# Kernel optimization log

Measured on AMD Instinct MI355X. Metric: run time of the kernel, lower is better.

The kernel has to match this reference:

```python
import math
import jax, jax.numpy as jnp
import numpy as np

NUM_ANGLE = 8
NUM_RADIAL = 3
RADIAL_MIN = 0.08
RADIAL_MAX = 0.9
EPS = 1e-6


def _hann(n):
    # torch.hann_window(n, periodic=False)
    return 0.5 * (1.0 - jnp.cos(2.0 * jnp.pi * jnp.arange(n, dtype=jnp.float32) / (n - 1)))


def _to_luma(img):
    # img: [B, 3, H, W] -> [B, H, W]
    return 0.2989 * img[:, 0] + 0.587 * img[:, 1] + 0.114 * img[:, 2]


def _log_magnitude(img):
    x = _to_luma(img).astype(jnp.float32)  # [B, H, W]
    H, W = x.shape[-2], x.shape[-1]
    win = _hann(H)[:, None] * _hann(W)[None, :]  # [H, W]
    x = x * win
    spec = jnp.fft.fftshift(jnp.fft.fft2(x, axes=(-2, -1)), axes=(-2, -1))
    return jnp.log1p(jnp.abs(spec))  # [B, H, W]


def _polar_masks(H, W):
    y = jnp.linspace(-1.0, 1.0, H, dtype=jnp.float32)
    x = jnp.linspace(-1.0, 1.0, W, dtype=jnp.float32)
    yy, xx = jnp.meshgrid(y, x, indexing='ij')
    radius = jnp.sqrt(xx * xx + yy * yy)
    radius = radius / jnp.maximum(radius.max(), EPS)
    angle = jnp.remainder(jnp.arctan2(yy, xx), math.pi)

    r_edges = jnp.linspace(RADIAL_MIN, RADIAL_MAX, NUM_RADIAL + 1, dtype=jnp.float32)
    a_edges = jnp.linspace(0.0, math.pi, NUM_ANGLE + 1, dtype=jnp.float32)

    r0 = r_edges[:-1][:, None, None]
    r1 = r_edges[1:][:, None, None]
    rmask = (radius[None] >= r0) & (radius[None] < r1)           # [R, H, W]
    rmask = rmask.at[-1].set((radius >= r_edges[-2]) & (radius <= r_edges[-1]))

    t0 = a_edges[:-1][:, None, None]
    t1 = a_edges[1:][:, None, None]
    amask = (angle[None] >= t0) & (angle[None] < t1)             # [A, H, W]
    amask = amask.at[-1].set((angle >= a_edges[-2]) & (angle <= a_edges[-1]))

    return (rmask[:, None] & amask[None, :]).astype(jnp.float32)  # [R, A, H, W]


def _sector_energies(img):
    mag = _log_magnitude(img)                          # [B, H, W]
    masks = _polar_masks(mag.shape[-2], mag.shape[-1])  # [R, A, H, W]
    mask_sum = jnp.maximum(masks.sum(axis=(-2, -1)), EPS)        # [R, A]
    masked_sum = jnp.einsum('bhw,rahw->bra', mag, masks)         # [B, R, A]
    energies = masked_sum / mask_sum[None]
    energies = energies / jnp.maximum(energies.sum(axis=-1, keepdims=True), EPS)
    return energies


def setup_inputs() -> dict:
    key = jax.random.key(0)
    k1, k2 = jax.random.split(key)
    B, C, H, W = 16, 3, 512, 512
    prediction = jax.random.uniform(k1, (B, C, H, W), dtype=jnp.float32)
    target = jax.random.uniform(k2, (B, C, H, W), dtype=jnp.float32)
    radial_weights = jnp.array([0.5, 1.0, 1.2], dtype=jnp.float32).reshape(1, NUM_RADIAL, 1)
    return {"prediction": prediction, "target": target, "radial_weights": radial_weights}


def reference(prediction, target, radial_weights):
    pred_e = _sector_energies(prediction)   # [B, R, A]
    tgt_e = _sector_energies(target)
    diff = pred_e - tgt_e
    dist = jnp.sqrt(diff * diff + EPS)      # charbonnier
    return (dist * radial_weights).mean()
```

## Files before the change

kernel.cpp:

```cpp
#include <hip/hip_runtime.h>
#include <math.h>

#define PI_F 3.14159265358979323846f
#define TWO_PI_F 6.28318530717958647692f
#define RSQ2 0.70710678118654752440f

#define LGKM(n) __asm__ volatile("s_waitcnt lgkmcnt(" #n ")" ::: "memory")
#define LADDR(a) ((a) + ((a) >> 3))

__device__ __forceinline__ float2 cadd(float2 a, float2 b){ return make_float2(a.x+b.x, a.y+b.y); }
__device__ __forceinline__ float2 csub(float2 a, float2 b){ return make_float2(a.x-b.x, a.y-b.y); }
__device__ __forceinline__ float2 cmul(float2 a, float2 b){ return make_float2(a.x*b.x - a.y*b.y, a.x*b.y + a.y*b.x); }
__device__ __forceinline__ float2 cw1(float2 a){ return make_float2(RSQ2*(a.x+a.y), RSQ2*(a.y-a.x)); }
__device__ __forceinline__ float2 cw2(float2 a){ return make_float2(a.y, -a.x); }
__device__ __forceinline__ float2 cw3(float2 a){ return make_float2(RSQ2*(a.y-a.x), -RSQ2*(a.x+a.y)); }

__device__ __forceinline__ void dft8(float2* v){
    float2 a0=cadd(v[0],v[4]), a1=cadd(v[1],v[5]), a2=cadd(v[2],v[6]), a3=cadd(v[3],v[7]);
    float2 b0=csub(v[0],v[4]);
    float2 b1=cw1(csub(v[1],v[5]));
    float2 b2=cw2(csub(v[2],v[6]));
    float2 b3=cw3(csub(v[3],v[7]));
    float2 c0=cadd(a0,a2), c2=csub(a0,a2), c1=cadd(a1,a3), c3=cw2(csub(a1,a3));
    float2 d0=cadd(b0,b2), d2=csub(b0,b2), d1=cadd(b1,b3), d3=cw2(csub(b1,b3));
    v[0]=cadd(c0,c1); v[1]=csub(c0,c1);
    v[2]=cadd(c2,c3); v[3]=csub(c2,c3);
    v[4]=cadd(d0,d1); v[5]=csub(d0,d1);
    v[6]=cadd(d2,d3); v[7]=csub(d2,d3);
}

__device__ __forceinline__ void calc_pows(float2 w, float2* p){
    p[0] = w;
    p[1] = cmul(w, w);
    p[2] = cmul(p[1], w);
    p[3] = cmul(p[1], p[1]);
    p[4] = cmul(p[2], p[1]);
    p[5] = cmul(p[2], p[2]);
    p[6] = cmul(p[3], p[2]);
}

__device__ __forceinline__ void stage_store(float2* wl, const float2* v, const float2* p,
                                            int base, int step){
    constexpr int br[8] = {0,4,2,6,1,5,3,7};
    wl[LADDR(base)] = v[0];
    #pragma unroll
    for (int c = 1; c < 8; ++c) wl[LADDR(base + step*c)] = cmul(v[br[c]], p[c-1]);
}

__device__ __forceinline__ void stage_load(const float2* wl, float2* v, int j){
    #pragma unroll
    for (int i = 0; i < 8; ++i) v[i] = wl[LADDR(j + 64*i)];
}

__device__ __forceinline__ int sector_id(int hm, int wm) {
    const float step = 2.0f / 511.0f;
    float y = -1.0f + step * (float)hm;
    float x = -1.0f + step * (float)wm;
    float radius = sqrtf(x * x + y * y);
    float r = radius / sqrtf(2.0f);
    float a = atan2f(y, x);
    a = fmodf(a, PI_F);
    if (a < 0.0f) a += PI_F;

    const float rstep = (0.9f - 0.08f) / 3.0f;
    const float re0 = 0.08f;
    const float re1 = 0.08f + rstep;
    const float re2 = 0.08f + 2.0f * rstep;
    const float re3 = 0.9f;
    int rb;
    if      (r >= re0 && r < re1)  rb = 0;
    else if (r >= re1 && r < re2)  rb = 1;
    else if (r >= re2 && r <= re3) rb = 2;
    else return -1;

    const float astep = PI_F / 8.0f;
    int ab = 7;
    #pragma unroll
    for (int i = 0; i < 7; ++i) {
        float t0 = astep * (float)i;
        float t1 = astep * (float)(i + 1);
        if (a >= t0 && a < t1) { ab = i; break; }
    }
    return rb * 8 + ab;
}

__device__ __forceinline__ float hannf(int i) {
    return 0.5f * (1.0f - __cosf(TWO_PI_F * (float)i / 511.0f));
}

__device__ __forceinline__ float lumaf(const float* b, size_t off){
    return 0.2989f*b[off] + 0.587f*b[off+262144] + 0.114f*b[off+524288];
}

__global__ __launch_bounds__(256, 4) void rowfft_kernel(const float* __restrict__ pred,
                                                        const float* __restrict__ tgt,
                                                        float4* __restrict__ out4,
                                                        unsigned char* __restrict__ mapT,
                                                        unsigned short* __restrict__ cnt_u16,
                                                        float* __restrict__ acc_rep) {
    __shared__ float2 lds[4 * 1152];
    __shared__ float cbins[24];
    int blk = blockIdx.x;
    int img = blk >> 5;
    int pb  = blk & 31;
    int t = threadIdx.x;
    int wv = t >> 6, j = t & 63;
    int hpA = pb * 8 + wv * 2;
    int hpB = hpA + 1;
    int h0 = 2 * hpA;
    float2* wlA = lds + wv * 1152;
    float2* wlB = wlA + 576;

    if (blk < 48) acc_rep[blk * 256 + t] = 0.0f;
    if (t < 24) cbins[t] = 0.0f;
    __syncthreads();
    {
        int idx = blk * 256 + t;
        int wm = idx >> 9, hm = idx & 511;
        int s = sector_id(hm, wm);
        mapT[idx] = (unsigned char)(s < 0 ? 255 : s);
        if (s >= 0) atomicAdd(&cbins[s], 1.0f);
    }

    const float* base = (img < 16) ? (pred + (size_t)img * 786432)
                                   : (tgt  + (size_t)(img - 16) * 786432);
    float whA0 = hannf(h0), whA1 = hannf(h0 + 1);
    float whB0 = hannf(h0 + 2), whB1 = hannf(h0 + 3);
    float2 va[8], vb[8];
    #pragma unroll
    for (int i = 0; i < 8; ++i) {
        int w = j + 64 * i;
        float ww = hannf(w);
        size_t off0 = (size_t)h0 * 512 + w;
        float l0 = lumaf(base, off0);
        float l1 = lumaf(base, off0 + 512);
        float l2 = lumaf(base, off0 + 1024);
        float l3 = lumaf(base, off0 + 1536);
        va[i] = make_float2(l0 * (whA0 * ww), l1 * (whA1 * ww));
        vb[i] = make_float2(l2 * (whB0 * ww), l3 * (whB1 * ww));
    }

    float sn, cs;
    __sincosf(-TWO_PI_F * (float)j / 512.0f, &sn, &cs);
    float2 tw0 = make_float2(cs, sn);
    __sincosf(-TWO_PI_F * (float)((j >> 3) << 3) / 512.0f, &sn, &cs);
    float2 tw1 = make_float2(cs, sn);
    float2 pw[7];

    calc_pows(tw0, pw);
    dft8(va);
    dft8(vb);
    stage_store(wlA, va, pw, 8 * j, 1);
    stage_store(wlB, vb, pw, 8 * j, 1);
    LGKM(8);
    stage_load(wlA, va, j);
    LGKM(8);
    stage_load(wlB, vb, j);
    LGKM(8);
    calc_pows(tw1, pw);
    dft8(va);
    stage_store(wlA, va, pw, (j & 7) + 64 * (j >> 3), 8);
    LGKM(8);
    dft8(vb);
    stage_store(wlB, vb, pw, (j & 7) + 64 * (j >> 3), 8);
    LGKM(8);
    stage_load(wlA, va, j);
    LGKM(8);
    stage_load(wlB, vb, j);
    LGKM(8);
    dft8(va);
    LGKM(0);
    dft8(vb);

    constexpr int br[8] = {0,4,2,6,1,5,3,7};
    size_t kbase = (size_t)img * 256;
    int partner = (64 - j) & 63;
    #pragma unroll
    for (int c = 0; c < 4; ++c) {
        int k = j + 64 * c;
        float2 zk = va[br[c]];
        float mx = __shfl(va[br[7 - c]].x, partner, 64);
        float my = __shfl(va[br[7 - c]].y, partner, 64);
        float2 zs = va[br[(8 - c) & 7]];
        float2 zm = make_float2(j == 0 ? zs.x : mx, j == 0 ? zs.y : my);
        float4 o = make_float4(0.5f*(zk.x+zm.x), 0.5f*(zk.y-zm.y),
                               0.5f*(zk.y+zm.y), 0.5f*(zm.x-zk.x));
        if (k != 0) out4[(kbase + (size_t)k) * 256 + hpA] = o;
        zk = vb[br[c]];
        mx = __shfl(vb[br[7 - c]].x, partner, 64);
        my = __shfl(vb[br[7 - c]].y, partner, 64);
        zs = vb[br[(8 - c) & 7]];
        zm = make_float2(j == 0 ? zs.x : mx, j == 0 ? zs.y : my);
        o = make_float4(0.5f*(zk.x+zm.x), 0.5f*(zk.y-zm.y),
                        0.5f*(zk.y+zm.y), 0.5f*(zm.x-zk.x));
        if (k != 0) out4[(kbase + (size_t)k) * 256 + hpB] = o;
    }
    if (j == 0) {
        float2 z0 = va[br[0]], z4 = va[br[4]];
        out4[kbase * 256 + hpA] = make_float4(z0.x, z4.x, z0.y, z4.y);
        z0 = vb[br[0]]; z4 = vb[br[4]];
        out4[kbase * 256 + hpB] = make_float4(z0.x, z4.x, z0.y, z4.y);
    }
    __syncthreads();
    if (t < 24) cnt_u16[t * 1024 + blk] = (unsigned short)(int)cbins[t];
}

__global__ __launch_bounds__(256, 4) void colfft_kernel(const float2* __restrict__ buf,
                                                        const unsigned char* __restrict__ mapT,
                                                        float* __restrict__ acc_rep) {
    __shared__ float2 lds[4 * 1152];
    int t = threadIdx.x;
    int wv = t >> 6, j = t & 63;
    int pg = blockIdx.x * 4 + wv;
    int gidA = pg * 2;
    int img = pg >> 7;
    int wA = gidA & 255, wB = wA + 1;
    float2* wlA = lds + wv * 1152;
    float2* wlB = wlA + 576;

    const float2* colA = buf + (size_t)gidA * 512;
    float2 va[8], vb[8];
    #pragma unroll
    for (int i = 0; i < 8; ++i) va[i] = colA[j + 64 * i];
    #pragma unroll
    for (int i = 0; i < 8; ++i) vb[i] = colA[512 + j + 64 * i];

    bool pairw = (wA == 0);
    const unsigned char* mwA1 = mapT + (size_t)(pairw ? 256 : ((wA + 256) & 511)) * 512;
    const unsigned char* mwA2 = mapT + (size_t)(pairw ? 0   : ((256 - wA) & 511)) * 512;
    const unsigned char* mwB1 = mapT + (size_t)((wB + 256) & 511) * 512;
    const unsigned char* mwB2 = mapT + (size_t)((256 - wB) & 511) * 512;
    unsigned char sA1[8], sA2[8], sB1[8], sB2[8];
    #pragma unroll
    for (int c = 0; c < 8; ++c) {
        int hm = j + 64 * ((c + 4) & 7);
        int hm2 = (256 - (j + 64 * c)) & 511;
        sA1[c] = mwA1[hm];
        sA2[c] = pairw ? mwA2[hm] : mwA2[hm2];
        sB1[c] = mwB1[hm];
        sB2[c] = mwB2[hm2];
    }

    float sn, cs;
    __sincosf(-TWO_PI_F * (float)j / 512.0f, &sn, &cs);
    float2 tw0 = make_float2(cs, sn);
    __sincosf(-TWO_PI_F * (float)((j >> 3) << 3) / 512.0f, &sn, &cs);
    float2 tw1 = make_float2(cs, sn);
    float2 pw[7];

    calc_pows(tw0, pw);
    dft8(va);
    dft8(vb);
    stage_store(wlA, va, pw, 8 * j, 1);
    stage_store(wlB, vb, pw, 8 * j, 1);
    LGKM(8);
    stage_load(wlA, va, j);
    LGKM(8);
    stage_load(wlB, vb, j);
    LGKM(8);
    calc_pows(tw1, pw);
    dft8(va);
    stage_store(wlA, va, pw, (j & 7) + 64 * (j >> 3), 8);
    LGKM(8);
    dft8(vb);
    stage_store(wlB, vb, pw, (j & 7) + 64 * (j >> 3), 8);
    LGKM(8);
    stage_load(wlA, va, j);
    LGKM(8);
    stage_load(wlB, vb, j);
    LGKM(8);
    dft8(va);
    LGKM(0);
    dft8(vb);

    float* wb = (float*)wlA;
    #pragma unroll
    for (int i = 0; i < 4; ++i) { int ii = j + 64 * i; if (ii < 200) wb[ii] = 0.0f; }
    LGKM(0);

    constexpr int br[8] = {0,4,2,6,1,5,3,7};
    int rep = (j & 7) * 25;
    if (pairw) {
        int partner = (64 - j) & 63;
        #pragma unroll
        for (int c = 0; c < 8; ++c) {
            float2 zk = va[br[c]];
            float mx = __shfl(va[br[7 - c]].x, partner, 64);
            float my = __shfl(va[br[7 - c]].y, partner, 64);
            float2 zs = va[br[(8 - c) & 7]];
            float2 zm = make_float2(j == 0 ? zs.x : mx, j == 0 ? zs.y : my);
            float f0x = 0.5f*(zk.x+zm.x), f0y = 0.5f*(zk.y-zm.y);
            float f1x = 0.5f*(zk.y+zm.y), f1y = 0.5f*(zm.x-zk.x);
            float mag0 = __logf(1.0f + sqrtf(f0x*f0x + f0y*f0y));
            float mag1 = __logf(1.0f + sqrtf(f1x*f1x + f1y*f1y));
            int s1 = sA1[c]; if (s1 < 24) atomicAdd(&wb[rep + s1], mag0);
            int s2 = sA2[c]; if (s2 < 24) atomicAdd(&wb[rep + s2], mag1);
        }
    } else {
        #pragma unroll
        for (int c = 0; c < 8; ++c) {
            float2 z = va[br[c]];
            float mag = __logf(1.0f + sqrtf(z.x * z.x + z.y * z.y));
            int s1 = sA1[c]; if (s1 < 24) atomicAdd(&wb[rep + s1], mag);
            int s2 = sA2[c]; if (s2 < 24) atomicAdd(&wb[rep + s2], mag);
        }
    }
    #pragma unroll
    for (int c = 0; c < 8; ++c) {
        float2 z = vb[br[c]];
        float mag = __logf(1.0f + sqrtf(z.x * z.x + z.y * z.y));
        int s1 = sB1[c]; if (s1 < 24) atomicAdd(&wb[rep + s1], mag);
        int s2 = sB2[c]; if (s2 < 24) atomicAdd(&wb[rep + s2], mag);
    }
    LGKM(0);
    if (j < 24) {
        float sum = 0.0f;
        #pragma unroll
        for (int r = 0; r < 8; ++r) sum += wb[r * 25 + j];
        atomicAdd(&acc_rep[(pg & 15) * 768 + img * 24 + j], sum);
    }
}

__global__ __launch_bounds__(256) void final_kernel(const float* __restrict__ acc_rep,
                                                    const unsigned short* __restrict__ cnt_u16,
                                                    const float* __restrict__ rw,
                                                    float* __restrict__ out) {
    __shared__ float accs[768];
    __shared__ float cnts[24];
    __shared__ float ep[384], et[384], red[384];
    int t = threadIdx.x;
    for (int o = t; o < 768; o += 256) {
        float s = 0.0f;
        #pragma unroll
        for (int r = 0; r < 16; ++r) s += acc_rep[r * 768 + o];
        accs[o] = s;
    }
    if (t < 192) {
        int s = t >> 3, g = t & 7;
        const ushort4* p = (const ushort4*)(cnt_u16 + s * 1024 + g * 128);
        float sum = 0.0f;
        #pragma unroll
        for (int i = 0; i < 32; ++i) { ushort4 u = p[i]; sum += (float)(u.x + u.y + u.z + u.w); }
        sum += __shfl_down(sum, 4, 8);
        sum += __shfl_down(sum, 2, 8);
        sum += __shfl_down(sum, 1, 8);
        if (g == 0) cnts[s] = sum;
    }
    __syncthreads();
    for (int idx = t; idx < 384; idx += 256) {
        int b = idx / 24, s = idx - b * 24;
        float cnt = fmaxf(cnts[s], 1e-6f);
        ep[idx] = accs[b * 24 + s] / cnt;
        et[idx] = accs[(16 + b) * 24 + s] / cnt;
    }
    __syncthreads();
    for (int idx = t; idx < 384; idx += 256) {
        int b = idx / 24, s = idx - b * 24, r = s >> 3;
        int gbase = b * 24 + r * 8;
        float sp = 0.0f, st = 0.0f;
        #pragma unroll
        for (int a = 0; a < 8; ++a) { sp += ep[gbase + a]; st += et[gbase + a]; }
        float pe = ep[idx] / fmaxf(sp, 1e-6f);
        float te = et[idx] / fmaxf(st, 1e-6f);
        float d = pe - te;
        red[idx] = sqrtf(d * d + 1e-6f) * rw[r];
    }
    __syncthreads();
    if (t < 128) red[t] += red[t + 128] + red[t + 256];
    __syncthreads();
    if (t < 64) {
        float vv = red[t] + red[t + 64];
        #pragma unroll
        for (int o = 32; o > 0; o >>= 1) vv += __shfl_down(vv, o, 64);
        if (t == 0) out[0] = vv / 384.0f;
    }
}

extern "C" void kernel_launch(void* const* d_in, const int* in_sizes, int n_in,
                              void* d_out, int out_size, void* d_ws, size_t ws_size,
                              hipStream_t stream) {
    const float* pred = (const float*)d_in[0];
    const float* tgt  = (const float*)d_in[1];
    const float* rw   = (const float*)d_in[2];

    char* ws = (char*)d_ws;
    float* acc_rep       = (float*)ws;
    unsigned short* cnt  = (unsigned short*)(ws + 49152);
    unsigned char* mapT  = (unsigned char*)(ws + 98304);
    float2* buf          = (float2*)(ws + 360448);

    rowfft_kernel<<<1024, 256, 0, stream>>>(pred, tgt, (float4*)buf, mapT, cnt, acc_rep);
    colfft_kernel<<<1024, 256, 0, stream>>>(buf, mapT, acc_rep);
    final_kernel<<<1, 256, 0, stream>>>(acc_rep, cnt, rw, (float*)d_out);
}
```

Before: 194.3 us.

## Use 512-thread blocks with interleaved image mapping and single-buffer column LDS

```diff
diff --git a/kernel.cpp b/kernel.cpp
--- a/kernel.cpp
+++ b/kernel.cpp
@@ -92,33 +92,37 @@
     return 0.2989f*b[off] + 0.587f*b[off+262144] + 0.114f*b[off+524288];
 }
 
-__global__ __launch_bounds__(256, 4) void rowfft_kernel(const float* __restrict__ pred,
+__device__ __forceinline__ void decode_blk(int blk, int& img, int& sub){
+    img = (blk & 7) * 4 + ((blk >> 3) & 3);
+    sub = blk >> 5;
+}
+
+__global__ __launch_bounds__(512, 4) void rowfft_kernel(const float* __restrict__ pred,
                                                         const float* __restrict__ tgt,
                                                         float4* __restrict__ out4,
                                                         unsigned char* __restrict__ mapT,
                                                         unsigned short* __restrict__ cnt_u16,
                                                         float* __restrict__ acc_rep) {
-    __shared__ float2 lds[4 * 1152];
+    __shared__ float2 lds[8 * 1152];
     __shared__ float cbins[24];
     int blk = blockIdx.x;
-    int img = blk >> 5;
-    int pb  = blk & 31;
+    int img, pb;
+    decode_blk(blk, img, pb);
     int t = threadIdx.x;
     int wv = t >> 6, j = t & 63;
-    int hpA = pb * 8 + wv * 2;
+    int hpA = pb * 16 + wv * 2;
     int hpB = hpA + 1;
     int h0 = 2 * hpA;
     float2* wlA = lds + wv * 1152;
     float2* wlB = wlA + 576;
 
-    if (blk < 48) acc_rep[blk * 256 + t] = 0.0f;
+    if (blk < 24) acc_rep[blk * 512 + t] = 0.0f;
     if (t < 24) cbins[t] = 0.0f;
     __syncthreads();
     {
-        int idx = blk * 256 + t;
-        int wm = idx >> 9, hm = idx & 511;
+        int wm = blk, hm = t;
         int s = sector_id(hm, wm);
-        mapT[idx] = (unsigned char)(s < 0 ? 255 : s);
+        mapT[blk * 512 + t] = (unsigned char)(s < 0 ? 255 : s);
         if (s >= 0) atomicAdd(&cbins[s], 1.0f);
     }
 
@@ -202,23 +206,23 @@
         out4[kbase * 256 + hpB] = make_float4(z0.x, z4.x, z0.y, z4.y);
     }
     __syncthreads();
-    if (t < 24) cnt_u16[t * 1024 + blk] = (unsigned short)(int)cbins[t];
-}
-
-__global__ __launch_bounds__(256, 4) void colfft_kernel(const float2* __restrict__ buf,
+    if (t < 24) cnt_u16[t * 512 + blk] = (unsigned short)(int)cbins[t];
+}
+
+__global__ __launch_bounds__(512, 6) void colfft_kernel(const float2* __restrict__ buf,
                                                         const unsigned char* __restrict__ mapT,
                                                         float* __restrict__ acc_rep) {
-    __shared__ float2 lds[4 * 1152];
+    __shared__ float2 lds[8 * 576];
+    int blk = blockIdx.x;
+    int img, cg;
+    decode_blk(blk, img, cg);
     int t = threadIdx.x;
     int wv = t >> 6, j = t & 63;
-    int pg = blockIdx.x * 4 + wv;
-    int gidA = pg * 2;
-    int img = pg >> 7;
-    int wA = gidA & 255, wB = wA + 1;
-    float2* wlA = lds + wv * 1152;
-    float2* wlB = wlA + 576;
-
-    const float2* colA = buf + (size_t)gidA * 512;
+    int pl = cg * 8 + wv;
+    int wA = 2 * pl, wB = wA + 1;
+    float2* wl = lds + wv * 576;
+
+    const float2* colA = buf + (size_t)(img * 256 + wA) * 512;
     float2 va[8], vb[8];
     #pragma unroll
     for (int i = 0; i < 8; ++i) va[i] = colA[j + 64 * i];
@@ -250,38 +254,38 @@
 
     calc_pows(tw0, pw);
     dft8(va);
-    dft8(vb);
-    stage_store(wlA, va, pw, 8 * j, 1);
-    stage_store(wlB, vb, pw, 8 * j, 1);
-    LGKM(8);
-    stage_load(wlA, va, j);
-    LGKM(8);
-    stage_load(wlB, vb, j);
-    LGKM(8);
+    stage_store(wl, va, pw, 8 * j, 1);
+    dft8(vb);
+    LGKM(0);
+    stage_load(wl, va, j);
+    LGKM(0);
+    stage_store(wl, vb, pw, 8 * j, 1);
     calc_pows(tw1, pw);
     dft8(va);
-    stage_store(wlA, va, pw, (j & 7) + 64 * (j >> 3), 8);
-    LGKM(8);
-    dft8(vb);
-    stage_store(wlB, vb, pw, (j & 7) + 64 * (j >> 3), 8);
-    LGKM(8);
-    stage_load(wlA, va, j);
-    LGKM(8);
-    stage_load(wlB, vb, j);
-    LGKM(8);
-    dft8(va);
-    LGKM(0);
-    dft8(vb);
-
-    float* wb = (float*)wlA;
+    LGKM(0);
+    stage_load(wl, vb, j);
+    LGKM(0);
+    stage_store(wl, va, pw, (j & 7) + 64 * (j >> 3), 8);
+    dft8(vb);
+    LGKM(0);
+    stage_load(wl, va, j);
+    LGKM(0);
+    stage_store(wl, vb, pw, (j & 7) + 64 * (j >> 3), 8);
+    dft8(va);
+    LGKM(0);
+    stage_load(wl, vb, j);
+    LGKM(0);
+    dft8(vb);
+
+    float* wb = (float*)wl;
     #pragma unroll
     for (int i = 0; i < 4; ++i) { int ii = j + 64 * i; if (ii < 200) wb[ii] = 0.0f; }
     LGKM(0);
 
     constexpr int br[8] = {0,4,2,6,1,5,3,7};
+    int partner = (64 - j) & 63;
     int rep = (j & 7) * 25;
     if (pairw) {
-        int partner = (64 - j) & 63;
         #pragma unroll
         for (int c = 0; c < 8; ++c) {
             float2 zk = va[br[c]];
@@ -317,7 +321,7 @@
         float sum = 0.0f;
         #pragma unroll
         for (int r = 0; r < 8; ++r) sum += wb[r * 25 + j];
-        atomicAdd(&acc_rep[(pg & 15) * 768 + img * 24 + j], sum);
+        atomicAdd(&acc_rep[(pl & 15) * 768 + img * 24 + j], sum);
     }
 }
 
@@ -337,10 +341,10 @@
     }
     if (t < 192) {
         int s = t >> 3, g = t & 7;
-        const ushort4* p = (const ushort4*)(cnt_u16 + s * 1024 + g * 128);
+        const ushort4* p = (const ushort4*)(cnt_u16 + s * 512 + g * 64);
         float sum = 0.0f;
         #pragma unroll
-        for (int i = 0; i < 32; ++i) { ushort4 u = p[i]; sum += (float)(u.x + u.y + u.z + u.w); }
+        for (int i = 0; i < 16; ++i) { ushort4 u = p[i]; sum += (float)(u.x + u.y + u.z + u.w); }
         sum += __shfl_down(sum, 4, 8);
         sum += __shfl_down(sum, 2, 8);
         sum += __shfl_down(sum, 1, 8);
@@ -389,7 +393,7 @@
     unsigned char* mapT  = (unsigned char*)(ws + 98304);
     float2* buf          = (float2*)(ws + 360448);
 
-    rowfft_kernel<<<1024, 256, 0, stream>>>(pred, tgt, (float4*)buf, mapT, cnt, acc_rep);
-    colfft_kernel<<<1024, 256, 0, stream>>>(buf, mapT, acc_rep);
+    rowfft_kernel<<<512, 512, 0, stream>>>(pred, tgt, (float4*)buf, mapT, cnt, acc_rep);
+    colfft_kernel<<<512, 512, 0, stream>>>(buf, mapT, acc_rep);
     final_kernel<<<1, 256, 0, stream>>>(acc_rep, cnt, rw, (float*)d_out);
 }
```

New measurement: 200.4 us. 3.1% more time.

## Fuse row FFT, column FFT and final reduction into one persistent kernel

Applied to the files above, without the earlier changes.

```diff
diff --git a/kernel.cpp b/kernel.cpp
--- a/kernel.cpp
+++ b/kernel.cpp
@@ -7,6 +7,8 @@
 
 #define LGKM(n) __asm__ volatile("s_waitcnt lgkmcnt(" #n ")" ::: "memory")
 #define LADDR(a) ((a) + ((a) >> 3))
+
+#define NBLK 512u
 
 __device__ __forceinline__ float2 cadd(float2 a, float2 b){ return make_float2(a.x+b.x, a.y+b.y); }
 __device__ __forceinline__ float2 csub(float2 a, float2 b){ return make_float2(a.x-b.x, a.y-b.y); }
@@ -92,54 +94,36 @@
     return 0.2989f*b[off] + 0.587f*b[off+262144] + 0.114f*b[off+524288];
 }
 
-__global__ __launch_bounds__(256, 4) void rowfft_kernel(const float* __restrict__ pred,
-                                                        const float* __restrict__ tgt,
-                                                        float4* __restrict__ out4,
-                                                        unsigned char* __restrict__ mapT,
-                                                        unsigned short* __restrict__ cnt_u16,
-                                                        float* __restrict__ acc_rep) {
-    __shared__ float2 lds[4 * 1152];
+__device__ __forceinline__ void grid_barrier(unsigned* ctr){
+    __syncthreads();
+    if (threadIdx.x == 0) {
+        __threadfence();
+        __hip_atomic_fetch_add(ctr, 1u, __ATOMIC_RELEASE, __HIP_MEMORY_SCOPE_AGENT);
+        while (__hip_atomic_load(ctr, __ATOMIC_ACQUIRE, __HIP_MEMORY_SCOPE_AGENT) < NBLK)
+            __builtin_amdgcn_s_sleep(2);
+        __threadfence();
+    }
+    __syncthreads();
+}
+
+__global__ __launch_bounds__(512, 4) void fused_kernel(const float* __restrict__ pred,
+                                                       const float* __restrict__ tgt,
+                                                       float2* buf,
+                                                       unsigned char* __restrict__ mapT,
+                                                       unsigned short* __restrict__ cnt_u16,
+                                                       float* __restrict__ acc_rep,
+                                                       const float* __restrict__ rw,
+                                                       float* __restrict__ out,
+                                                       unsigned* ctrs) {
+    __shared__ float2 lds[8 * 1152];
     __shared__ float cbins[24];
     int blk = blockIdx.x;
-    int img = blk >> 5;
-    int pb  = blk & 31;
     int t = threadIdx.x;
     int wv = t >> 6, j = t & 63;
-    int hpA = pb * 8 + wv * 2;
-    int hpB = hpA + 1;
-    int h0 = 2 * hpA;
+    constexpr int br[8] = {0,4,2,6,1,5,3,7};
+    int partner = (64 - j) & 63;
     float2* wlA = lds + wv * 1152;
     float2* wlB = wlA + 576;
-
-    if (blk < 48) acc_rep[blk * 256 + t] = 0.0f;
-    if (t < 24) cbins[t] = 0.0f;
-    __syncthreads();
-    {
-        int idx = blk * 256 + t;
-        int wm = idx >> 9, hm = idx & 511;
-        int s = sector_id(hm, wm);
-        mapT[idx] = (unsigned char)(s < 0 ? 255 : s);
-        if (s >= 0) atomicAdd(&cbins[s], 1.0f);
-    }
-
-    const float* base = (img < 16) ? (pred + (size_t)img * 786432)
-                                   : (tgt  + (size_t)(img - 16) * 786432);
-    float whA0 = hannf(h0), whA1 = hannf(h0 + 1);
-    float whB0 = hannf(h0 + 2), whB1 = hannf(h0 + 3);
-    float2 va[8], vb[8];
-    #pragma unroll
-    for (int i = 0; i < 8; ++i) {
-        int w = j + 64 * i;
-        float ww = hannf(w);
-        size_t off0 = (size_t)h0 * 512 + w;
-        float l0 = lumaf(base, off0);
-        float l1 = lumaf(base, off0 + 512);
-        float l2 = lumaf(base, off0 + 1024);
-        float l3 = lumaf(base, off0 + 1536);
-        va[i] = make_float2(l0 * (whA0 * ww), l1 * (whA1 * ww));
-        vb[i] = make_float2(l2 * (whB0 * ww), l3 * (whB1 * ww));
-    }
-
     float sn, cs;
     __sincosf(-TWO_PI_F * (float)j / 512.0f, &sn, &cs);
     float2 tw0 = make_float2(cs, sn);
@@ -147,232 +131,253 @@
     float2 tw1 = make_float2(cs, sn);
     float2 pw[7];
 
-    calc_pows(tw0, pw);
-    dft8(va);
-    dft8(vb);
-    stage_store(wlA, va, pw, 8 * j, 1);
-    stage_store(wlB, vb, pw, 8 * j, 1);
-    LGKM(8);
-    stage_load(wlA, va, j);
-    LGKM(8);
-    stage_load(wlB, vb, j);
-    LGKM(8);
-    calc_pows(tw1, pw);
-    dft8(va);
-    stage_store(wlA, va, pw, (j & 7) + 64 * (j >> 3), 8);
-    LGKM(8);
-    dft8(vb);
-    stage_store(wlB, vb, pw, (j & 7) + 64 * (j >> 3), 8);
-    LGKM(8);
-    stage_load(wlA, va, j);
-    LGKM(8);
-    stage_load(wlB, vb, j);
-    LGKM(8);
-    dft8(va);
-    LGKM(0);
-    dft8(vb);
-
-    constexpr int br[8] = {0,4,2,6,1,5,3,7};
-    size_t kbase = (size_t)img * 256;
-    int partner = (64 - j) & 63;
-    #pragma unroll
-    for (int c = 0; c < 4; ++c) {
-        int k = j + 64 * c;
-        float2 zk = va[br[c]];
-        float mx = __shfl(va[br[7 - c]].x, partner, 64);
-        float my = __shfl(va[br[7 - c]].y, partner, 64);
-        float2 zs = va[br[(8 - c) & 7]];
-        float2 zm = make_float2(j == 0 ? zs.x : mx, j == 0 ? zs.y : my);
-        float4 o = make_float4(0.5f*(zk.x+zm.x), 0.5f*(zk.y-zm.y),
-                               0.5f*(zk.y+zm.y), 0.5f*(zm.x-zk.x));
-        if (k != 0) out4[(kbase + (size_t)k) * 256 + hpA] = o;
-        zk = vb[br[c]];
-        mx = __shfl(vb[br[7 - c]].x, partner, 64);
-        my = __shfl(vb[br[7 - c]].y, partner, 64);
-        zs = vb[br[(8 - c) & 7]];
-        zm = make_float2(j == 0 ? zs.x : mx, j == 0 ? zs.y : my);
-        o = make_float4(0.5f*(zk.x+zm.x), 0.5f*(zk.y-zm.y),
-                        0.5f*(zk.y+zm.y), 0.5f*(zm.x-zk.x));
-        if (k != 0) out4[(kbase + (size_t)k) * 256 + hpB] = o;
-    }
-    if (j == 0) {
-        float2 z0 = va[br[0]], z4 = va[br[4]];
-        out4[kbase * 256 + hpA] = make_float4(z0.x, z4.x, z0.y, z4.y);
-        z0 = vb[br[0]]; z4 = vb[br[4]];
-        out4[kbase * 256 + hpB] = make_float4(z0.x, z4.x, z0.y, z4.y);
-    }
-    __syncthreads();
-    if (t < 24) cnt_u16[t * 1024 + blk] = (unsigned short)(int)cbins[t];
-}
-
-__global__ __launch_bounds__(256, 4) void colfft_kernel(const float2* __restrict__ buf,
-                                                        const unsigned char* __restrict__ mapT,
-                                                        float* __restrict__ acc_rep) {
-    __shared__ float2 lds[4 * 1152];
-    int t = threadIdx.x;
-    int wv = t >> 6, j = t & 63;
-    int pg = blockIdx.x * 4 + wv;
-    int gidA = pg * 2;
-    int img = pg >> 7;
-    int wA = gidA & 255, wB = wA + 1;
-    float2* wlA = lds + wv * 1152;
-    float2* wlB = wlA + 576;
-
-    const float2* colA = buf + (size_t)gidA * 512;
-    float2 va[8], vb[8];
-    #pragma unroll
-    for (int i = 0; i < 8; ++i) va[i] = colA[j + 64 * i];
-    #pragma unroll
-    for (int i = 0; i < 8; ++i) vb[i] = colA[512 + j + 64 * i];
-
-    bool pairw = (wA == 0);
-    const unsigned char* mwA1 = mapT + (size_t)(pairw ? 256 : ((wA + 256) & 511)) * 512;
-    const unsigned char* mwA2 = mapT + (size_t)(pairw ? 0   : ((256 - wA) & 511)) * 512;
-    const unsigned char* mwB1 = mapT + (size_t)((wB + 256) & 511) * 512;
-    const unsigned char* mwB2 = mapT + (size_t)((256 - wB) & 511) * 512;
-    unsigned char sA1[8], sA2[8], sB1[8], sB2[8];
-    #pragma unroll
-    for (int c = 0; c < 8; ++c) {
-        int hm = j + 64 * ((c + 4) & 7);
-        int hm2 = (256 - (j + 64 * c)) & 511;
-        sA1[c] = mwA1[hm];
-        sA2[c] = pairw ? mwA2[hm] : mwA2[hm2];
-        sB1[c] = mwB1[hm];
-        sB2[c] = mwB2[hm2];
-    }
-
-    float sn, cs;
-    __sincosf(-TWO_PI_F * (float)j / 512.0f, &sn, &cs);
-    float2 tw0 = make_float2(cs, sn);
-    __sincosf(-TWO_PI_F * (float)((j >> 3) << 3) / 512.0f, &sn, &cs);
-    float2 tw1 = make_float2(cs, sn);
-    float2 pw[7];
-
-    calc_pows(tw0, pw);
-    dft8(va);
-    dft8(vb);
-    stage_store(wlA, va, pw, 8 * j, 1);
-    stage_store(wlB, vb, pw, 8 * j, 1);
-    LGKM(8);
-    stage_load(wlA, va, j);
-    LGKM(8);
-    stage_load(wlB, vb, j);
-    LGKM(8);
-    calc_pows(tw1, pw);
-    dft8(va);
-    stage_store(wlA, va, pw, (j & 7) + 64 * (j >> 3), 8);
-    LGKM(8);
-    dft8(vb);
-    stage_store(wlB, vb, pw, (j & 7) + 64 * (j >> 3), 8);
-    LGKM(8);
-    stage_load(wlA, va, j);
-    LGKM(8);
-    stage_load(wlB, vb, j);
-    LGKM(8);
-    dft8(va);
-    LGKM(0);
-    dft8(vb);
-
-    float* wb = (float*)wlA;
-    #pragma unroll
-    for (int i = 0; i < 4; ++i) { int ii = j + 64 * i; if (ii < 200) wb[ii] = 0.0f; }
-    LGKM(0);
-
-    constexpr int br[8] = {0,4,2,6,1,5,3,7};
-    int rep = (j & 7) * 25;
-    if (pairw) {
-        int partner = (64 - j) & 63;
-        #pragma unroll
-        for (int c = 0; c < 8; ++c) {
+    {
+        int img = blk >> 4;
+        int pb  = blk & 15;
+        int hpA = pb * 16 + wv * 2;
+        int hpB = hpA + 1;
+        int h0 = 2 * hpA;
+        float4* out4 = (float4*)buf;
+
+        if (blk < 24) acc_rep[blk * 512 + t] = 0.0f;
+        if (t < 24) cbins[t] = 0.0f;
+        __syncthreads();
+        {
+            int wm = blk, hm = t;
+            int s = sector_id(hm, wm);
+            mapT[blk * 512 + t] = (unsigned char)(s < 0 ? 255 : s);
+            if (s >= 0) atomicAdd(&cbins[s], 1.0f);
+        }
+
+        const float* base = (img < 16) ? (pred + (size_t)img * 786432)
+                                       : (tgt  + (size_t)(img - 16) * 786432);
+        float whA0 = hannf(h0), whA1 = hannf(h0 + 1);
+        float whB0 = hannf(h0 + 2), whB1 = hannf(h0 + 3);
+        float2 va[8], vb[8];
+        #pragma unroll
+        for (int i = 0; i < 8; ++i) {
+            int w = j + 64 * i;
+            float ww = hannf(w);
+            size_t off0 = (size_t)h0 * 512 + w;
+            float l0 = lumaf(base, off0);
+            float l1 = lumaf(base, off0 + 512);
+            float l2 = lumaf(base, off0 + 1024);
+            float l3 = lumaf(base, off0 + 1536);
+            va[i] = make_float2(l0 * (whA0 * ww), l1 * (whA1 * ww));
+            vb[i] = make_float2(l2 * (whB0 * ww), l3 * (whB1 * ww));
+        }
+
+        calc_pows(tw0, pw);
+        dft8(va);
+        dft8(vb);
+        stage_store(wlA, va, pw, 8 * j, 1);
+        stage_store(wlB, vb, pw, 8 * j, 1);
+        LGKM(8);
+        stage_load(wlA, va, j);
+        LGKM(8);
+        stage_load(wlB, vb, j);
+        LGKM(8);
+        calc_pows(tw1, pw);
+        dft8(va);
+        stage_store(wlA, va, pw, (j & 7) + 64 * (j >> 3), 8);
+        LGKM(8);
+        dft8(vb);
+        stage_store(wlB, vb, pw, (j & 7) + 64 * (j >> 3), 8);
+        LGKM(8);
+        stage_load(wlA, va, j);
+        LGKM(8);
+        stage_load(wlB, vb, j);
+        LGKM(8);
+        dft8(va);
+        LGKM(0);
+        dft8(vb);
+
+        size_t kbase = (size_t)img * 256;
+        #pragma unroll
+        for (int c = 0; c < 4; ++c) {
+            int k = j + 64 * c;
             float2 zk = va[br[c]];
             float mx = __shfl(va[br[7 - c]].x, partner, 64);
             float my = __shfl(va[br[7 - c]].y, partner, 64);
             float2 zs = va[br[(8 - c) & 7]];
             float2 zm = make_float2(j == 0 ? zs.x : mx, j == 0 ? zs.y : my);
-            float f0x = 0.5f*(zk.x+zm.x), f0y = 0.5f*(zk.y-zm.y);
-            float f1x = 0.5f*(zk.y+zm.y), f1y = 0.5f*(zm.x-zk.x);
-            float mag0 = __logf(1.0f + sqrtf(f0x*f0x + f0y*f0y));
-            float mag1 = __logf(1.0f + sqrtf(f1x*f1x + f1y*f1y));
-            int s1 = sA1[c]; if (s1 < 24) atomicAdd(&wb[rep + s1], mag0);
-            int s2 = sA2[c]; if (s2 < 24) atomicAdd(&wb[rep + s2], mag1);
-        }
-    } else {
+            float4 o = make_float4(0.5f*(zk.x+zm.x), 0.5f*(zk.y-zm.y),
+                                   0.5f*(zk.y+zm.y), 0.5f*(zm.x-zk.x));
+            if (k != 0) out4[(kbase + (size_t)k) * 256 + hpA] = o;
+            zk = vb[br[c]];
+            mx = __shfl(vb[br[7 - c]].x, partner, 64);
+            my = __shfl(vb[br[7 - c]].y, partner, 64);
+            zs = vb[br[(8 - c) & 7]];
+            zm = make_float2(j == 0 ? zs.x : mx, j == 0 ? zs.y : my);
+            o = make_float4(0.5f*(zk.x+zm.x), 0.5f*(zk.y-zm.y),
+                            0.5f*(zk.y+zm.y), 0.5f*(zm.x-zk.x));
+            if (k != 0) out4[(kbase + (size_t)k) * 256 + hpB] = o;
+        }
+        if (j == 0) {
+            float2 z0 = va[br[0]], z4 = va[br[4]];
+            out4[kbase * 256 + hpA] = make_float4(z0.x, z4.x, z0.y, z4.y);
+            z0 = vb[br[0]]; z4 = vb[br[4]];
+            out4[kbase * 256 + hpB] = make_float4(z0.x, z4.x, z0.y, z4.y);
+        }
+        __syncthreads();
+        if (t < 24) cnt_u16[t * 512 + blk] = (unsigned short)(int)cbins[t];
+    }
+
+    grid_barrier(&ctrs[0]);
+
+    {
+        int img = blk >> 4;
+        int cg  = blk & 15;
+        int pl = cg * 8 + wv;
+        int wA = 2 * pl, wB = wA + 1;
+
+        const float2* colA = buf + (size_t)(img * 256 + wA) * 512;
+        float2 va[8], vb[8];
+        #pragma unroll
+        for (int i = 0; i < 8; ++i) va[i] = colA[j + 64 * i];
+        #pragma unroll
+        for (int i = 0; i < 8; ++i) vb[i] = colA[512 + j + 64 * i];
+
+        bool pairw = (wA == 0);
+        const unsigned char* mwA1 = mapT + (size_t)(pairw ? 256 : ((wA + 256) & 511)) * 512;
+        const unsigned char* mwA2 = mapT + (size_t)(pairw ? 0   : ((256 - wA) & 511)) * 512;
+        const unsigned char* mwB1 = mapT + (size_t)((wB + 256) & 511) * 512;
+        const unsigned char* mwB2 = mapT + (size_t)((256 - wB) & 511) * 512;
+        unsigned char sA1[8], sA2[8], sB1[8], sB2[8];
         #pragma unroll
         for (int c = 0; c < 8; ++c) {
-            float2 z = va[br[c]];
+            int hm = j + 64 * ((c + 4) & 7);
+            int hm2 = (256 - (j + 64 * c)) & 511;
+            sA1[c] = mwA1[hm];
+            sA2[c] = pairw ? mwA2[hm] : mwA2[hm2];
+            sB1[c] = mwB1[hm];
+            sB2[c] = mwB2[hm2];
+        }
+
+        calc_pows(tw0, pw);
+        dft8(va);
+        dft8(vb);
+        stage_store(wlA, va, pw, 8 * j, 1);
+        stage_store(wlB, vb, pw, 8 * j, 1);
+        LGKM(8);
+        stage_load(wlA, va, j);
+        LGKM(8);
+        stage_load(wlB, vb, j);
+        LGKM(8);
+        calc_pows(tw1, pw);
+        dft8(va);
+        stage_store(wlA, va, pw, (j & 7) + 64 * (j >> 3), 8);
+        LGKM(8);
+        dft8(vb);
+        stage_store(wlB, vb, pw, (j & 7) + 64 * (j >> 3), 8);
+        LGKM(8);
+        stage_load(wlA, va, j);
+        LGKM(8);
+        stage_load(wlB, vb, j);
+        LGKM(8);
+        dft8(va);
+        LGKM(0);
+        dft8(vb);
+
+        float* wb = (float*)wlA;
+        #pragma unroll
+        for (int i = 0; i < 4; ++i) { int ii = j + 64 * i; if (ii < 200) wb[ii] = 0.0f; }
+        LGKM(0);
+
+        int rep = (j & 7) * 25;
+        if (pairw) {
+            #pragma unroll
+            for (int c = 0; c < 8; ++c) {
+                float2 zk = va[br[c]];
+                float mx = __shfl(va[br[7 - c]].x, partner, 64);
+                float my = __shfl(va[br[7 - c]].y, partner, 64);
+                float2 zs = va[br[(8 - c) & 7]];
+                float2 zm = make_float2(j == 0 ? zs.x : mx, j == 0 ? zs.y : my);
+                float f0x = 0.5f*(zk.x+zm.x), f0y = 0.5f*(zk.y-zm.y);
+                float f1x = 0.5f*(zk.y+zm.y), f1y = 0.5f*(zm.x-zk.x);
+                float mag0 = __logf(1.0f + sqrtf(f0x*f0x + f0y*f0y));
+                float mag1 = __logf(1.0f + sqrtf(f1x*f1x + f1y*f1y));
+                int s1 = sA1[c]; if (s1 < 24) atomicAdd(&wb[rep + s1], mag0);
+                int s2 = sA2[c]; if (s2 < 24) atomicAdd(&wb[rep + s2], mag1);
+            }
+        } else {
+            #pragma unroll
+            for (int c = 0; c < 8; ++c) {
+                float2 z = va[br[c]];
+                float mag = __logf(1.0f + sqrtf(z.x * z.x + z.y * z.y));
+                int s1 = sA1[c]; if (s1 < 24) atomicAdd(&wb[rep + s1], mag);
+                int s2 = sA2[c]; if (s2 < 24) atomicAdd(&wb[rep + s2], mag);
+            }
+        }
+        #pragma unroll
+        for (int c = 0; c < 8; ++c) {
+            float2 z = vb[br[c]];
             float mag = __logf(1.0f + sqrtf(z.x * z.x + z.y * z.y));
-            int s1 = sA1[c]; if (s1 < 24) atomicAdd(&wb[rep + s1], mag);
-            int s2 = sA2[c]; if (s2 < 24) atomicAdd(&wb[rep + s2], mag);
+            int s1 = sB1[c]; if (s1 < 24) atomicAdd(&wb[rep + s1], mag);
+            int s2 = sB2[c]; if (s2 < 24) atomicAdd(&wb[rep + s2], mag);
+        }
+        LGKM(0);
+        if (j < 24) {
+            float sum = 0.0f;
+            #pragma unroll
+            for (int r = 0; r < 8; ++r) sum += wb[r * 25 + j];
+            atomicAdd(&acc_rep[(pl & 15) * 768 + img * 24 + j], sum);
         }
     }
-    #pragma unroll
-    for (int c = 0; c < 8; ++c) {
-        float2 z = vb[br[c]];
-        float mag = __logf(1.0f + sqrtf(z.x * z.x + z.y * z.y));
-        int s1 = sB1[c]; if (s1 < 24) atomicAdd(&wb[rep + s1], mag);
-        int s2 = sB2[c]; if (s2 < 24) atomicAdd(&wb[rep + s2], mag);
-    }
-    LGKM(0);
-    if (j < 24) {
-        float sum = 0.0f;
-        #pragma unroll
-        for (int r = 0; r < 8; ++r) sum += wb[r * 25 + j];
-        atomicAdd(&acc_rep[(pg & 15) * 768 + img * 24 + j], sum);
-    }
-}
-
-__global__ __launch_bounds__(256) void final_kernel(const float* __restrict__ acc_rep,
-                                                    const unsigned short* __restrict__ cnt_u16,
-                                                    const float* __restrict__ rw,
-                                                    float* __restrict__ out) {
-    __shared__ float accs[768];
-    __shared__ float cnts[24];
-    __shared__ float ep[384], et[384], red[384];
-    int t = threadIdx.x;
-    for (int o = t; o < 768; o += 256) {
-        float s = 0.0f;
-        #pragma unroll
-        for (int r = 0; r < 16; ++r) s += acc_rep[r * 768 + o];
-        accs[o] = s;
-    }
-    if (t < 192) {
-        int s = t >> 3, g = t & 7;
-        const ushort4* p = (const ushort4*)(cnt_u16 + s * 1024 + g * 128);
-        float sum = 0.0f;
-        #pragma unroll
-        for (int i = 0; i < 32; ++i) { ushort4 u = p[i]; sum += (float)(u.x + u.y + u.z + u.w); }
-        sum += __shfl_down(sum, 4, 8);
-        sum += __shfl_down(sum, 2, 8);
-        sum += __shfl_down(sum, 1, 8);
-        if (g == 0) cnts[s] = sum;
-    }
-    __syncthreads();
-    for (int idx = t; idx < 384; idx += 256) {
-        int b = idx / 24, s = idx - b * 24;
-        float cnt = fmaxf(cnts[s], 1e-6f);
-        ep[idx] = accs[b * 24 + s] / cnt;
-        et[idx] = accs[(16 + b) * 24 + s] / cnt;
-    }
-    __syncthreads();
-    for (int idx = t; idx < 384; idx += 256) {
-        int b = idx / 24, s = idx - b * 24, r = s >> 3;
-        int gbase = b * 24 + r * 8;
-        float sp = 0.0f, st = 0.0f;
-        #pragma unroll
-        for (int a = 0; a < 8; ++a) { sp += ep[gbase + a]; st += et[gbase + a]; }
-        float pe = ep[idx] / fmaxf(sp, 1e-6f);
-        float te = et[idx] / fmaxf(st, 1e-6f);
-        float d = pe - te;
-        red[idx] = sqrtf(d * d + 1e-6f) * rw[r];
-    }
-    __syncthreads();
-    if (t < 128) red[t] += red[t + 128] + red[t + 256];
-    __syncthreads();
-    if (t < 64) {
-        float vv = red[t] + red[t + 64];
-        #pragma unroll
-        for (int o = 32; o > 0; o >>= 1) vv += __shfl_down(vv, o, 64);
-        if (t == 0) out[0] = vv / 384.0f;
+
+    grid_barrier(&ctrs[1]);
+
+    if (blk == 0) {
+        float* f0   = (float*)lds;
+        float* cnts = f0 + 768;
+        float* ep   = f0 + 800;
+        float* et   = f0 + 1184;
+        float* red  = f0 + 1568;
+        for (int o = t; o < 768; o += 512) {
+            float s = 0.0f;
+            #pragma unroll
+            for (int r = 0; r < 16; ++r) s += acc_rep[r * 768 + o];
+            f0[o] = s;
+        }
+        if (t < 192) {
+            int s = t >> 3, g = t & 7;
+            const ushort4* p = (const ushort4*)(cnt_u16 + s * 512 + g * 64);
+            float sum = 0.0f;
+            #pragma unroll
+            for (int i = 0; i < 16; ++i) { ushort4 u = p[i]; sum += (float)(u.x + u.y + u.z + u.w); }
+            sum += __shfl_down(sum, 4, 8);
+            sum += __shfl_down(sum, 2, 8);
+            sum += __shfl_down(sum, 1, 8);
+            if (g == 0) cnts[s] = sum;
+        }
+        __syncthreads();
+        if (t < 384) {
+            int b = t / 24, s = t - b * 24;
+            float cnt = fmaxf(cnts[s], 1e-6f);
+            ep[t] = f0[b * 24 + s] / cnt;
+            et[t] = f0[(16 + b) * 24 + s] / cnt;
+        }
+        __syncthreads();
+        if (t < 384) {
+            int b = t / 24, s = t - b * 24, r = s >> 3;
+            int gbase = b * 24 + r * 8;
+            float sp = 0.0f, st = 0.0f;
+            #pragma unroll
+            for (int a = 0; a < 8; ++a) { sp += ep[gbase + a]; st += et[gbase + a]; }
+            float pe = ep[t] / fmaxf(sp, 1e-6f);
+            float te = et[t] / fmaxf(st, 1e-6f);
+            float d = pe - te;
+            red[t] = sqrtf(d * d + 1e-6f) * rw[r];
+        }
+        __syncthreads();
+        if (t < 128) red[t] += red[t + 128] + red[t + 256];
+        __syncthreads();
+        if (t < 64) {
+            float vv = red[t] + red[t + 64];
+            #pragma unroll
+            for (int o = 32; o > 0; o >>= 1) vv += __shfl_down(vv, o, 64);
+            if (t == 0) out[0] = vv / 384.0f;
+        }
     }
 }
 
@@ -386,10 +391,12 @@
     char* ws = (char*)d_ws;
     float* acc_rep       = (float*)ws;
     unsigned short* cnt  = (unsigned short*)(ws + 49152);
+    unsigned* ctrs       = (unsigned*)(ws + 73728);
     unsigned char* mapT  = (unsigned char*)(ws + 98304);
     float2* buf          = (float2*)(ws + 360448);
-
-    rowfft_kernel<<<1024, 256, 0, stream>>>(pred, tgt, (float4*)buf, mapT, cnt, acc_rep);
-    colfft_kernel<<<1024, 256, 0, stream>>>(buf, mapT, acc_rep);
-    final_kernel<<<1, 256, 0, stream>>>(acc_rep, cnt, rw, (float*)d_out);
-}
+    float* outp          = (float*)d_out;
+
+    hipMemsetAsync(ctrs, 0, 2 * sizeof(unsigned), stream);
+    fused_kernel<<<NBLK, 512, 0, stream>>>(pred, tgt, buf, mapT, cnt, acc_rep,
+                                           rw, outp, ctrs);
+}
```

Result: slower. 377.5 us (+94.3%).
